# Performance work log

Hardware: AMD Instinct MI355X
Metric: run time of the kernel (lower is better)

Reference implementation:

```python
import jax, jax.numpy as jnp
import numpy as np

EPS = 1e-12  # F.normalize eps


def setup_inputs() -> dict:
    key = jax.random.key(0)
    ks = jax.random.split(key, 6)
    B, T, D = 8, 4096, 1024
    L, K, CD = 8, 1024, 16
    return {
        "z_e": jax.random.normal(ks[0], (B, T, D), jnp.float32),
        "Wd": jax.random.normal(ks[1], (L, CD, D), jnp.float32) * 0.02,
        "bd": jnp.zeros((L, CD), jnp.float32),
        "cb": jax.random.normal(ks[2], (L, K, CD), jnp.float32) * 0.02,
        "Wu": jax.random.normal(ks[3], (L, D, CD), jnp.float32) * 0.02,
        "bu": jnp.zeros((L, D), jnp.float32),
    }


def _l2norm(x):
    return x / jnp.maximum(jnp.linalg.norm(x, axis=-1, keepdims=True), EPS)


def reference(z_e, Wd, bd, cb, Wu, bu):
    """z_e: (B,T,D). Returns (z_q_concat, codes, commitment_loss, codebook_loss, entropy_loss)."""
    B, T, D = z_e.shape
    L, K, CD = cb.shape
    sg = jax.lax.stop_gradient
    residual = z_e
    zq_list, codes_list = [], []
    commit = jnp.asarray(0.0, z_e.dtype)
    cbl = jnp.asarray(0.0, z_e.dtype)
    for i in range(L):
        # proj_down: Linear(D -> CD), weight (CD, D)
        z_i = jnp.einsum('btd,cd->btc', residual, Wd[i]) + bd[i]  # (B,T,CD)
        flat = z_i.reshape(-1, CD)                                 # (N,CD)
        cb_i = cb[i]                                               # (K,CD)
        # L2-normalized lookup; argmin of euclidean cdist == argmin of squared dist
        zn, cbn = _l2norm(flat), _l2norm(cb_i)
        d2 = (jnp.sum(zn * zn, -1, keepdims=True)
              - 2.0 * (zn @ cbn.T)
              + jnp.sum(cbn * cbn, -1))                            # (N,K)
        codes = jnp.argmin(d2, axis=-1)                            # (N,)
        z_q = cb_i[codes].reshape(B, T, CD)                        # gather from RAW codebook
        commit = commit + jnp.mean((z_i - sg(z_q)) ** 2)
        cbl = cbl + jnp.mean((z_q - sg(z_i)) ** 2)
        zq_list.append(z_i + sg(z_q - z_i))                        # straight-through
        # residual update uses detached z_q; proj_up weight (D, CD)
        residual = residual - (jnp.einsum('btc,dc->btd', sg(z_q), Wu[i]) + bu[i])
        codes_list.append(codes.reshape(B, T))
    z_q_concat = jnp.concatenate(zq_list, axis=-1)                 # (B,T,L*CD)
    codes_all = jnp.stack(codes_list, axis=-1)                     # (B,T,L)
    entropy_loss = jnp.asarray(0.0, z_e.dtype)                     # entropy_loss_weight == 0
    return z_q_concat, codes_all, commit, cbl, entropy_loss
```

## Files before the change

### kernel.cpp

```cpp
#include <hip/hip_runtime.h>
#include <math.h>


#define TAU 3e-4f

#define WS_WACC   0
#define WS_HV64   64
#define WS_G64    2048
#define WS_CBN64  133120
#define WS_CBF    1247232
#define WS_G32    1902592
#define WS_HV32   1968128
#define WS_BMAT   1968640
#define WS_SBU    2492928

typedef __attribute__((ext_vector_type(8))) short short8v;
typedef __attribute__((ext_vector_type(4))) float f32x4;

__device__ __forceinline__ void gload_lds16(const void* g, void* l) {
    __builtin_amdgcn_global_load_lds(
        (const __attribute__((address_space(1))) void*)g,
        (__attribute__((address_space(3))) void*)l, 16, 0, 0);
}

__device__ __forceinline__ unsigned short bf16_rne(float x) {
    unsigned u = __float_as_uint(x);
    u += 0x7FFFu + ((u >> 16) & 1u);
    return (unsigned short)(u >> 16);
}
__device__ __forceinline__ float bf16_to_f32(unsigned short h) {
    return __uint_as_float(((unsigned)h) << 16);
}

__global__ void __launch_bounds__(256) rvq_prep1(
    const float* __restrict__ cb, const float* __restrict__ Wd,
    const float* __restrict__ bu,
    double* __restrict__ cbn64, unsigned short* __restrict__ cbf,
    float* __restrict__ Bmat, double* __restrict__ sbu,
    double* __restrict__ wacc)
{
    const int b = blockIdx.x, t = threadIdx.x;
    if (b < 32) {
        const int idx = b * 256 + t;
        const float* cp = cb + (size_t)idx * 16;
        double v[16]; double n = 0.0;
#pragma unroll
        for (int c = 0; c < 16; ++c) { v[c] = (double)cp[c]; n = fma(v[c], v[c], n); }
        const double iv = 1.0 / fmax(sqrt(n), 1e-12);
        double* r64 = cbn64 + (size_t)idx * 17;
        unsigned short* cf = cbf + (size_t)idx * 32;
        double c2 = 0.0;
#pragma unroll
        for (int c = 0; c < 16; ++c) {
            const double x = v[c] * iv;
            c2 = fma(x, x, c2);
            r64[c] = x;
            const float xf = (float)x;
            const unsigned short hh = bf16_rne(xf);
            cf[c] = hh;
            cf[16 + c] = bf16_rne(xf - bf16_to_f32(hh));
        }
        r64[16] = c2;
    } else if (b < 160) {
        const int ic = b - 32;
        const int d0 = t * 4;
        const float4 v = *(const float4*)(Wd + (size_t)ic * 1024 + d0);
        Bmat[(size_t)(d0 + 0) * 128 + ic] = v.x;
        Bmat[(size_t)(d0 + 1) * 128 + ic] = v.y;
        Bmat[(size_t)(d0 + 2) * 128 + ic] = v.z;
        Bmat[(size_t)(d0 + 3) * 128 + ic] = v.w;
    } else if (b < 192) {
        const int idx = b - 160;
        const int i = idx >> 2, d = (idx & 3) * 256 + t;
        double s = 0.0;
        for (int j = 0; j < i; ++j) s += (double)bu[j * 1024 + d];
        sbu[i * 1024 + d] = s;
    } else {
        if (t == 0) wacc[0] = 0.0;
    }
}

__global__ void __launch_bounds__(256) rvq_prep2(
    const float* __restrict__ Wu, const float* __restrict__ Wd,
    const float* __restrict__ bd, const double* __restrict__ sbu,
    double* __restrict__ G64, float* __restrict__ G32,
    double* __restrict__ hv64, float* __restrict__ hv32)
{
    __shared__ double sm2[1200];
    float* smf = (float*)sm2;
    const int b = blockIdx.x, t = threadIdx.x;
    if (b < 64) {
        const int j = b >> 3, i = b & 7;
        if (j >= i) return;
        float* Aus = smf;
        float* Bds = smf + 1280;
        const int a = t >> 4, bb = t & 15;
        double s = 0.0;
        for (int ch = 0; ch < 16; ++ch) {
            __syncthreads();
            {
                const int dd = t >> 2, a4 = (t & 3) * 4;
                const float4 v = *(const float4*)(Wu + (size_t)j * 16384
                                  + (size_t)(ch * 64 + dd) * 16 + a4);
                *(float4*)&Aus[dd * 20 + a4] = v;
                const int br = t >> 4, d4 = (t & 15) * 4;
                const float4 w = *(const float4*)(Wd + (size_t)i * 16384
                                  + (size_t)br * 1024 + ch * 64 + d4);
                *(float4*)&Bds[br * 68 + d4] = w;
            }
            __syncthreads();
#pragma unroll
            for (int dd = 0; dd < 64; ++dd)
                s = fma((double)Aus[dd * 20 + a], (double)Bds[bb * 68 + dd], s);
        }
        G64[(size_t)(j * 8 + i) * 256 + t] = s;
        G32[(size_t)(j * 8 + i) * 256 + t] = (float)s;
    } else {
        const int i = b - 64;
        const int dq = t >> 4, bb = t & 15;
        const double* sp = sbu + i * 1024 + dq * 64;
        const float*  wp = Wd + (size_t)i * 16384 + (size_t)bb * 1024 + dq * 64;
        double s = 0.0;
#pragma unroll
        for (int dd = 0; dd < 64; ++dd)
            s = fma(sp[dd], (double)wp[dd], s);
        sm2[dq * 20 + bb] = s;
        __syncthreads();
        if (t < 16) {
            double s2 = 0.0;
#pragma unroll
            for (int q = 0; q < 16; ++q) s2 += sm2[q * 20 + t];
            const double h = (double)bd[i * 16 + t] - s2;
            hv64[i * 16 + t] = h; hv32[i * 16 + t] = (float)h;
        }
    }
}

__global__ void __launch_bounds__(256, 4) rvq_main(
    const float* __restrict__ z_e, const float* __restrict__ Wd,
    const float* __restrict__ cb,
    const float* __restrict__ Bmat, const float* __restrict__ hv32,
    const double* __restrict__ hv64,
    const unsigned short* __restrict__ cbf, const double* __restrict__ cbn64,
    const float* __restrict__ G32, const double* __restrict__ G64,
    double* __restrict__ wacc,
    float* __restrict__ out0, float* __restrict__ out1)
{
    __shared__ __attribute__((aligned(16))) double stag_d[1312];
    __shared__ float ybuf[32 * 132];
    __shared__ float znbuf[32 * 20];
    __shared__ float candd[64], candd2[64];
    __shared__ int   candk[64];
    __shared__ float zqs[32 * 17];
    __shared__ int   bkhist[256];
    __shared__ int   bks[32], flist[32];
    __shared__ int   flagcnt;
    float* stag = reinterpret_cast<float*>(stag_d);

    const int t = threadIdx.x;
    const int tok0g = blockIdx.x * 32;

    {
        float* As = stag;
        float* Bs = stag + 576;
        const int tg2 = t >> 5, cg2 = t & 31;
        const int wid = t >> 6, lane = t & 63;
        float acc[4][4];
#pragma unroll
        for (int h = 0; h < 4; ++h)
#pragma unroll
            for (int x = 0; x < 4; ++x) acc[h][x] = 0.f;

#pragma unroll 1
        for (int ko = 0; ko < 64; ++ko) {
            const int k0 = ko * 16;
            __syncthreads();
            {
                const int m = t >> 3, kk2 = (t & 7) * 2;
                const float2 v = *(const float2*)(z_e +
                    (size_t)(tok0g + m) * 1024 + k0 + kk2);
                As[kk2 * 36 + m] = v.x;
                As[(kk2 + 1) * 36 + m] = v.y;
            }
            {
                const float* bsrc = Bmat + (size_t)k0 * 128 + wid * 512 + lane * 4;
                float* bdst = Bs + wid * 512;
                gload_lds16(bsrc, bdst);
                gload_lds16(bsrc + 256, bdst + 256);
            }
            __syncthreads();
#pragma unroll
            for (int kk = 0; kk < 16; ++kk) {
                const float4 a4 = *(const float4*)&As[kk * 36 + tg2 * 4];
                const float4 b4 = *(const float4*)&Bs[kk * 128 + cg2 * 4];
                acc[0][0] = fmaf(a4.x, b4.x, acc[0][0]);
                acc[0][1] = fmaf(a4.x, b4.y, acc[0][1]);
                acc[0][2] = fmaf(a4.x, b4.z, acc[0][2]);
                acc[0][3] = fmaf(a4.x, b4.w, acc[0][3]);
                acc[1][0] = fmaf(a4.y, b4.x, acc[1][0]);
                acc[1][1] = fmaf(a4.y, b4.y, acc[1][1]);
                acc[1][2] = fmaf(a4.y, b4.z, acc[1][2]);
                acc[1][3] = fmaf(a4.y, b4.w, acc[1][3]);
                acc[2][0] = fmaf(a4.z, b4.x, acc[2][0]);
                acc[2][1] = fmaf(a4.z, b4.y, acc[2][1]);
                acc[2][2] = fmaf(a4.z, b4.z, acc[2][2]);
                acc[2][3] = fmaf(a4.z, b4.w, acc[2][3]);
                acc[3][0] = fmaf(a4.w, b4.x, acc[3][0]);
                acc[3][1] = fmaf(a4.w, b4.y, acc[3][1]);
                acc[3][2] = fmaf(a4.w, b4.z, acc[3][2]);
                acc[3][3] = fmaf(a4.w, b4.w, acc[3][3]);
            }
        }
        const float4 hv = *(const float4*)(hv32 + cg2 * 4);
#pragma unroll
        for (int h = 0; h < 4; ++h) {
            float4 y4;
            y4.x = acc[h][0] + hv.x;
            y4.y = acc[h][1] + hv.y;
            y4.z = acc[h][2] + hv.z;
            y4.w = acc[h][3] + hv.w;
            *(float4*)&ybuf[(tg2 * 4 + h) * 132 + cg2 * 4] = y4;
        }
    }

    double lacc = 0.0;
    const int w = t >> 6, lane = t & 63;
    const int blk = lane >> 4, col = lane & 15;
    const int Tt = w & 1, Hh = w >> 1;
    const bool lolane = blk >= 2;
#pragma unroll 1
    for (int l = 0; l < 8; ++l) {
        __syncthreads();
        if (t < 32) {
            const float* yr = &ybuf[t * 132 + l * 16];
            float yv[16]; float n2 = 0.f;
#pragma unroll
            for (int c = 0; c < 16; ++c) { yv[c] = yr[c]; n2 = fmaf(yv[c], yv[c], n2); }
            const float iv = 1.0f / fmaxf(sqrtf(n2), 1e-12f);
            float* zp = &znbuf[t * 20];
#pragma unroll
            for (int c = 0; c < 16; ++c) zp[c] = yv[c] * iv;
        }
        __syncthreads();

        short8v afrag;
        {
            const float* zp = &znbuf[(Tt * 16 + col) * 20 + (blk & 1) * 8];
            const float4 z0 = *(const float4*)zp;
            const float4 z1 = *(const float4*)(zp + 4);
            const float zv[8] = {z0.x, z0.y, z0.z, z0.w, z1.x, z1.y, z1.z, z1.w};
#pragma unroll
            for (int i = 0; i < 8; ++i) {
                const float x = -2.f * zv[i];
                const unsigned short h = bf16_rne(x);
                const unsigned short v2 = lolane ? bf16_rne(x - bf16_to_f32(h)) : h;
                afrag[i] = (short)v2;
            }
        }

        float bs[4], bs2[4]; int bk[4];
#pragma unroll
        for (int r = 0; r < 4; ++r) { bs[r] = 1e30f; bs2[r] = 1e30f; bk[r] = -1; }
        const unsigned short* cbp = cbf + ((size_t)(l * 1024 + Hh * 512 + col)) * 32;
        const unsigned short* p1 = cbp + (blk & 1) * 8;
        const unsigned short* p2 = cbp + 16 + (blk & 1) * 8;
#pragma unroll 2
        for (int tile = 0; tile < 32; ++tile) {
            const short8v b1 = *(const short8v*)(p1 + tile * 512);
            short8v b2 = {};
            if (!lolane) b2 = *(const short8v*)(p2 + tile * 512);
            f32x4 acc = {0.f, 0.f, 0.f, 0.f};
            acc = __builtin_amdgcn_mfma_f32_16x16x32_bf16(afrag, b1, acc, 0, 0, 0);
            acc = __builtin_amdgcn_mfma_f32_16x16x32_bf16(afrag, b2, acc, 0, 0, 0);
            const int k = Hh * 512 + tile * 16 + col;
#pragma unroll
            for (int r = 0; r < 4; ++r) {
                const float s = acc[r];
                const bool wn = s < bs[r];
                bs2[r] = wn ? bs[r] : fminf(bs2[r], s);
                bk[r]  = wn ? k : bk[r];
                bs[r]  = wn ? s : bs[r];
            }
        }

#pragma unroll
        for (int m = 1; m <= 8; m <<= 1) {
#pragma unroll
            for (int r = 0; r < 4; ++r) {
                const float ob = __shfl_xor(bs[r], m);
                const float os = __shfl_xor(bs2[r], m);
                const int   ok = __shfl_xor(bk[r], m);
                const bool wn = (ob < bs[r]) || (ob == bs[r] && ok < bk[r]);
                const float loser = wn ? bs[r] : ob;
                bs2[r] = fminf(fminf(bs2[r], os), loser);
                bs[r]  = wn ? ob : bs[r];
                bk[r]  = wn ? ok : bk[r];
            }
        }
        if (t == 0) flagcnt = 0;
        if (col == 0) {
#pragma unroll
            for (int r = 0; r < 4; ++r) {
                const int tok = Tt * 16 + blk * 4 + r;
                candd [Hh * 32 + tok] = bs[r];
                candd2[Hh * 32 + tok] = bs2[r];
                candk [Hh * 32 + tok] = bk[r];
            }
        }
        __syncthreads();
        if (t < 32) {
            float best = 1e30f, sec = 1e30f; int bkk = -1;
#pragma unroll
            for (int c = 0; c < 2; ++c) {
                const float d  = candd [c * 32 + t];
                const float d2 = candd2[c * 32 + t];
                const int   k  = candk [c * 32 + t];
                const bool wn = (d < best) || (d == best && k < bkk);
                const float nw = fminf(sec, fminf(best, d2));
                const float nl = fminf(sec, d);
                sec  = wn ? nw : nl;
                bkk  = wn ? k : bkk;
                best = wn ? d : best;
            }
            bks[t] = bkk;
            const float* yr = &ybuf[t * 132 + l * 16];
            float n2 = 0.f;
#pragma unroll
            for (int c = 0; c < 16; ++c) n2 = fmaf(yr[c], yr[c], n2);
            if ((sec - best < TAU) || (n2 < 1e-3f)) {
                const int p = atomicAdd(&flagcnt, 1); flist[p] = t;
            }
        }
        __syncthreads();

        const int nf = flagcnt;
#pragma unroll 1
        for (int f = 0; f < nf; ++f) {
            const int tok = flist[f];
            double* rpd = stag_d;
            {
                const int c = t & 15, ch = t >> 4;
                const float* gz = z_e + (size_t)(tok0g + tok) * 1024 + ch * 64;
                const float* wp = Wd + ((size_t)l * 16 + c) * 1024 + ch * 64;
                double pd = 0.0;
                for (int dd = 0; dd < 64; ++dd)
                    pd = fma((double)gz[dd], (double)wp[dd], pd);
                rpd[c * 16 + ch] = pd;
            }
            __syncthreads();
            if (t < 16) {
                double y = hv64[l * 16 + t];
#pragma unroll
                for (int ch = 0; ch < 16; ++ch) y += rpd[t * 16 + ch];
                for (int j = 0; j < l; ++j) {
                    const int bkj = bkhist[tok * 8 + j];
                    const float* qv = cb + ((size_t)j * 1024 + bkj) * 16;
                    const double* gp = G64 + (size_t)(j * 8 + l) * 256 + t;
                    double s = 0.0;
#pragma unroll
                    for (int a = 0; a < 16; ++a)
                        s = fma((double)qv[a], gp[a * 16], s);
                    y -= s;
                }
                rpd[256 + t] = y;
            }
            __syncthreads();
            if (t == 0) {
                double n2 = 0.0;
#pragma unroll
                for (int c = 0; c < 16; ++c) n2 = fma(rpd[256 + c], rpd[256 + c], n2);
                const double iv = 1.0 / fmax(sqrt(n2), 1e-12);
#pragma unroll
                for (int c = 0; c < 16; ++c) rpd[272 + c] = rpd[256 + c] * iv;
            }
            __syncthreads();
            {
                double bd_ = 1e300; int bk_ = -1;
#pragma unroll
                for (int q = 0; q < 4; ++q) {
                    const int k = q * 256 + t;
                    const double* row = cbn64 + (size_t)(l * 1024 + k) * 17;
                    double dot = 0.0;
#pragma unroll
                    for (int c = 0; c < 16; ++c) dot = fma(row[c], rpd[272 + c], dot);
                    const double s = fma(-2.0, dot, row[16]);
                    if (s < bd_) { bd_ = s; bk_ = k; }
                }
                rpd[288 + t] = bd_;
                ((int*)&rpd[544])[t] = bk_;
            }
            __syncthreads();
            if (t == 0) {
                double bd_ = 1e300; int bk_ = -1;
                for (int i = 0; i < 256; ++i) {
                    const double d = rpd[288 + i];
                    const int k = ((int*)&rpd[544])[i];
                    if (d < bd_ || (d == bd_ && k < bk_)) { bd_ = d; bk_ = k; }
                }
                bks[tok] = bk_;
            }
            __syncthreads();
        }

        if (t < 32) {
            const int bk_ = bks[t];
            bkhist[t * 8 + l] = bk_;
            const float4* qp = (const float4*)(cb + ((size_t)l * 1024 + bk_) * 16);
            const float4 q0 = qp[0], q1 = qp[1], q2 = qp[2], q3 = qp[3];
            float* op = out0 + (size_t)(tok0g + t) * 128 + l * 16;
            ((float4*)op)[0] = q0; ((float4*)op)[1] = q1;
            ((float4*)op)[2] = q2; ((float4*)op)[3] = q3;
            out1[(size_t)(tok0g + t) * 8 + l] = (float)bk_;
            const float qf[16] = {q0.x,q0.y,q0.z,q0.w, q1.x,q1.y,q1.z,q1.w,
                                  q2.x,q2.y,q2.z,q2.w, q3.x,q3.y,q3.z,q3.w};
#pragma unroll
            for (int a = 0; a < 16; ++a) zqs[t * 17 + a] = qf[a];
            const float* yr = &ybuf[t * 132 + l * 16];
#pragma unroll
            for (int c = 0; c < 16; ++c) {
                const float d = yr[c] - qf[c];
                lacc += (double)d * (double)d;
            }
        }
        __syncthreads();

        if (l < 7) {
            {
                const int total = (7 - l) * 256;
                for (int idx = t; idx < total; idx += 256) {
                    const int ii = l + 1 + (idx >> 8);
                    stag[idx] = G32[(size_t)(l * 8 + ii) * 256 + (idx & 255)];
                }
            }
            __syncthreads();
            const int part = t >> 5, tok = t & 31;
            const int ii = l + 1 + part;
            if (ii < 8) {
                float zql[16];
#pragma unroll
                for (int a = 0; a < 16; ++a) zql[a] = zqs[tok * 17 + a];
                const float* gb = &stag[part * 256];
                float corr[16];
#pragma unroll
                for (int x = 0; x < 16; ++x) corr[x] = 0.f;
#pragma unroll
                for (int a = 0; a < 16; ++a) {
                    const float4 g0 = *(const float4*)&gb[a * 16];
                    const float4 g1 = *(const float4*)&gb[a * 16 + 4];
                    const float4 g2 = *(const float4*)&gb[a * 16 + 8];
                    const float4 g3 = *(const float4*)&gb[a * 16 + 12];
                    const float za = zql[a];
                    corr[0]  = fmaf(za, g0.x, corr[0]);  corr[1]  = fmaf(za, g0.y, corr[1]);
                    corr[2]  = fmaf(za, g0.z, corr[2]);  corr[3]  = fmaf(za, g0.w, corr[3]);
                    corr[4]  = fmaf(za, g1.x, corr[4]);  corr[5]  = fmaf(za, g1.y, corr[5]);
                    corr[6]  = fmaf(za, g1.z, corr[6]);  corr[7]  = fmaf(za, g1.w, corr[7]);
                    corr[8]  = fmaf(za, g2.x, corr[8]);  corr[9]  = fmaf(za, g2.y, corr[9]);
                    corr[10] = fmaf(za, g2.z, corr[10]); corr[11] = fmaf(za, g2.w, corr[11]);
                    corr[12] = fmaf(za, g3.x, corr[12]); corr[13] = fmaf(za, g3.y, corr[13]);
                    corr[14] = fmaf(za, g3.z, corr[14]); corr[15] = fmaf(za, g3.w, corr[15]);
                }
                float* yr = &ybuf[tok * 132 + ii * 16];
#pragma unroll
                for (int v = 0; v < 4; ++v) {
                    float4 y4 = *(float4*)&yr[v * 4];
                    y4.x -= corr[v * 4 + 0]; y4.y -= corr[v * 4 + 1];
                    y4.z -= corr[v * 4 + 2]; y4.w -= corr[v * 4 + 3];
                    *(float4*)&yr[v * 4] = y4;
                }
            }
        }
    }

    if (t < 64) {
#pragma unroll
        for (int off = 32; off > 0; off >>= 1) lacc += __shfl_down(lacc, off);
        if (t == 0) atomicAdd(wacc, lacc);
    }
}

__global__ void __launch_bounds__(64) rvq_fin(const double* __restrict__ wacc,
                                              float* __restrict__ lossp) {
    if (threadIdx.x == 0) {
        const float v = (float)(wacc[0] * (1.0 / 524288.0));
        lossp[0] = v; lossp[1] = v; lossp[2] = 0.0f;
    }
}

extern "C" void kernel_launch(void* const* d_in, const int* in_sizes, int n_in,
                              void* d_out, int out_size, void* d_ws, size_t ws_size,
                              hipStream_t stream) {
    (void)in_sizes; (void)n_in; (void)ws_size;
    const float* z_e = (const float*)d_in[0];
    const float* Wd  = (const float*)d_in[1];
    const float* bd  = (const float*)d_in[2];
    const float* cb  = (const float*)d_in[3];
    const float* Wu  = (const float*)d_in[4];
    const float* bu  = (const float*)d_in[5];

    float* out0  = (float*)d_out;
    float* out1  = out0 + (size_t)8 * 4096 * 128;
    float* lossp = out0 + (size_t)out_size - 3;

    char* ws = (char*)d_ws;
    double* wacc  = (double*)(ws + WS_WACC);
    double* hv64  = (double*)(ws + WS_HV64);
    double* G64   = (double*)(ws + WS_G64);
    double* cbn64 = (double*)(ws + WS_CBN64);
    unsigned short* cbf = (unsigned short*)(ws + WS_CBF);
    float*  G32   = (float*) (ws + WS_G32);
    float*  hv32  = (float*) (ws + WS_HV32);
    float*  Bmat  = (float*) (ws + WS_BMAT);
    double* sbu   = (double*)(ws + WS_SBU);

    rvq_prep1<<<193, 256, 0, stream>>>(cb, Wd, bu, cbn64, cbf, Bmat, sbu, wacc);
    rvq_prep2<<<72, 256, 0, stream>>>(Wu, Wd, bd, sbu, G64, G32, hv64, hv32);
    rvq_main<<<1024, 256, 0, stream>>>(z_e, Wd, cb, Bmat, hv32, hv64,
                                       cbf, cbn64, G32, G64, wacc, out0, out1);
    rvq_fin<<<1, 64, 0, stream>>>(wacc, lossp);
}
```

Before: 658.2 us.

## Use split-bf16 MFMA for projection GEMM, merge prep kernels, widen search tiling

Replaces the fp32 FMA LDS-tiled projection GEMM (z_e x Wd^T) with MFMA 16x16x32 bf16 using a three-product hi/lo split, which keeps near-fp32 accuracy. Wd is pre-packed into bf16 hi/lo fragments, and z_e is read directly from global memory with no LDS staging. The two prep kernels are merged into one launch, and the sbu prefix sum is computed inline. Each wave in the codebook search now handles both 16-token halves over 256 codes instead of one half over 512, which reuses B fragments and removes the znbuf normalization pass and one barrier. The split-bf16 GEMM may shift near-tie results slightly, and the direct global loads of z_e are uncoalesced per lane.

After: 622.5 us. 5.4% less time.

```diff
diff --git a/kernel.cpp b/kernel.cpp
--- a/kernel.cpp
+++ b/kernel.cpp
@@ -11,17 +11,11 @@
 #define WS_CBF    1247232
 #define WS_G32    1902592
 #define WS_HV32   1968128
-#define WS_BMAT   1968640
-#define WS_SBU    2492928
+#define WS_BF     1968640
+#define BF_LO_OFF 131072
 
 typedef __attribute__((ext_vector_type(8))) short short8v;
 typedef __attribute__((ext_vector_type(4))) float f32x4;
-
-__device__ __forceinline__ void gload_lds16(const void* g, void* l) {
-    __builtin_amdgcn_global_load_lds(
-        (const __attribute__((address_space(1))) void*)g,
-        (__attribute__((address_space(3))) void*)l, 16, 0, 0);
-}
 
 __device__ __forceinline__ unsigned short bf16_rne(float x) {
     unsigned u = __float_as_uint(x);
@@ -32,13 +26,18 @@
     return __uint_as_float(((unsigned)h) << 16);
 }
 
-__global__ void __launch_bounds__(256) rvq_prep1(
+__global__ void __launch_bounds__(256) rvq_prep(
     const float* __restrict__ cb, const float* __restrict__ Wd,
+    const float* __restrict__ Wu, const float* __restrict__ bd,
     const float* __restrict__ bu,
     double* __restrict__ cbn64, unsigned short* __restrict__ cbf,
-    float* __restrict__ Bmat, double* __restrict__ sbu,
+    unsigned short* __restrict__ Bf,
+    double* __restrict__ G64, float* __restrict__ G32,
+    double* __restrict__ hv64, float* __restrict__ hv32,
     double* __restrict__ wacc)
 {
+    __shared__ double sm2[1200];
+    float* smf = (float*)sm2;
     const int b = blockIdx.x, t = threadIdx.x;
     if (b < 32) {
         const int idx = b * 256 + t;
@@ -61,36 +60,25 @@
             cf[16 + c] = bf16_rne(xf - bf16_to_f32(hh));
         }
         r64[16] = c2;
+    } else if (b < 96) {
+        const int u = (b - 32) * 4 + (t >> 6);
+        const int lane = t & 63;
+        const int ks = u >> 3, ctg = u & 7;
+        const int ic = ctg * 16 + (lane & 15);
+        const int kb = ks * 32 + (lane >> 4) * 8;
+        const float* wp = Wd + (size_t)ic * 1024 + kb;
+        const float4 w0 = *(const float4*)wp;
+        const float4 w1 = *(const float4*)(wp + 4);
+        const float wv[8] = {w0.x, w0.y, w0.z, w0.w, w1.x, w1.y, w1.z, w1.w};
+        unsigned short* dst = Bf + ((size_t)(ks * 8 + ctg) * 64 + lane) * 8;
+#pragma unroll
+        for (int i = 0; i < 8; ++i) {
+            const unsigned short hh = bf16_rne(wv[i]);
+            dst[i] = hh;
+            dst[BF_LO_OFF + i] = bf16_rne(wv[i] - bf16_to_f32(hh));
+        }
     } else if (b < 160) {
-        const int ic = b - 32;
-        const int d0 = t * 4;
-        const float4 v = *(const float4*)(Wd + (size_t)ic * 1024 + d0);
-        Bmat[(size_t)(d0 + 0) * 128 + ic] = v.x;
-        Bmat[(size_t)(d0 + 1) * 128 + ic] = v.y;
-        Bmat[(size_t)(d0 + 2) * 128 + ic] = v.z;
-        Bmat[(size_t)(d0 + 3) * 128 + ic] = v.w;
-    } else if (b < 192) {
-        const int idx = b - 160;
-        const int i = idx >> 2, d = (idx & 3) * 256 + t;
-        double s = 0.0;
-        for (int j = 0; j < i; ++j) s += (double)bu[j * 1024 + d];
-        sbu[i * 1024 + d] = s;
-    } else {
-        if (t == 0) wacc[0] = 0.0;
-    }
-}
-
-__global__ void __launch_bounds__(256) rvq_prep2(
-    const float* __restrict__ Wu, const float* __restrict__ Wd,
-    const float* __restrict__ bd, const double* __restrict__ sbu,
-    double* __restrict__ G64, float* __restrict__ G32,
-    double* __restrict__ hv64, float* __restrict__ hv32)
-{
-    __shared__ double sm2[1200];
-    float* smf = (float*)sm2;
-    const int b = blockIdx.x, t = threadIdx.x;
-    if (b < 64) {
-        const int j = b >> 3, i = b & 7;
+        const int j = (b - 96) >> 3, i = (b - 96) & 7;
         if (j >= i) return;
         float* Aus = smf;
         float* Bds = smf + 1280;
@@ -115,15 +103,17 @@
         }
         G64[(size_t)(j * 8 + i) * 256 + t] = s;
         G32[(size_t)(j * 8 + i) * 256 + t] = (float)s;
-    } else {
-        const int i = b - 64;
+    } else if (b < 168) {
+        const int i = b - 160;
         const int dq = t >> 4, bb = t & 15;
-        const double* sp = sbu + i * 1024 + dq * 64;
-        const float*  wp = Wd + (size_t)i * 16384 + (size_t)bb * 1024 + dq * 64;
+        const float* wp = Wd + (size_t)i * 16384 + (size_t)bb * 1024 + dq * 64;
+        const float* bup = bu + dq * 64;
         double s = 0.0;
-#pragma unroll
-        for (int dd = 0; dd < 64; ++dd)
-            s = fma(sp[dd], (double)wp[dd], s);
+        for (int dd = 0; dd < 64; ++dd) {
+            double sb = 0.0;
+            for (int j = 0; j < i; ++j) sb += (double)bup[j * 1024 + dd];
+            s = fma(sb, (double)wp[dd], s);
+        }
         sm2[dq * 20 + bb] = s;
         __syncthreads();
         if (t < 16) {
@@ -133,24 +123,25 @@
             const double h = (double)bd[i * 16 + t] - s2;
             hv64[i * 16 + t] = h; hv32[i * 16 + t] = (float)h;
         }
+    } else {
+        if (t == 0) wacc[0] = 0.0;
     }
 }
 
 __global__ void __launch_bounds__(256, 4) rvq_main(
     const float* __restrict__ z_e, const float* __restrict__ Wd,
     const float* __restrict__ cb,
-    const float* __restrict__ Bmat, const float* __restrict__ hv32,
+    const unsigned short* __restrict__ Bf, const float* __restrict__ hv32,
     const double* __restrict__ hv64,
     const unsigned short* __restrict__ cbf, const double* __restrict__ cbn64,
     const float* __restrict__ G32, const double* __restrict__ G64,
     double* __restrict__ wacc,
     float* __restrict__ out0, float* __restrict__ out1)
 {
-    __shared__ __attribute__((aligned(16))) double stag_d[1312];
+    __shared__ __attribute__((aligned(16))) double stag_d[896];
     __shared__ float ybuf[32 * 132];
-    __shared__ float znbuf[32 * 20];
-    __shared__ float candd[64], candd2[64];
-    __shared__ int   candk[64];
+    __shared__ float candd[128], candd2[128];
+    __shared__ int   candk[128];
     __shared__ float zqs[32 * 17];
     __shared__ int   bkhist[256];
     __shared__ int   bks[32], flist[32];
@@ -159,159 +150,141 @@
 
     const int t = threadIdx.x;
     const int tok0g = blockIdx.x * 32;
+    const int wq = t >> 6, lane = t & 63;
+    const int blk = lane >> 4, col = lane & 15, kh = blk & 1;
+    const bool lolane = blk >= 2;
 
     {
-        float* As = stag;
-        float* Bs = stag + 576;
-        const int tg2 = t >> 5, cg2 = t & 31;
-        const int wid = t >> 6, lane = t & 63;
-        float acc[4][4];
-#pragma unroll
-        for (int h = 0; h < 4; ++h)
-#pragma unroll
-            for (int x = 0; x < 4; ++x) acc[h][x] = 0.f;
-
-#pragma unroll 1
-        for (int ko = 0; ko < 64; ++ko) {
-            const int k0 = ko * 16;
-            __syncthreads();
-            {
-                const int m = t >> 3, kk2 = (t & 7) * 2;
-                const float2 v = *(const float2*)(z_e +
-                    (size_t)(tok0g + m) * 1024 + k0 + kk2);
-                As[kk2 * 36 + m] = v.x;
-                As[(kk2 + 1) * 36 + m] = v.y;
-            }
-            {
-                const float* bsrc = Bmat + (size_t)k0 * 128 + wid * 512 + lane * 4;
-                float* bdst = Bs + wid * 512;
-                gload_lds16(bsrc, bdst);
-                gload_lds16(bsrc + 256, bdst + 256);
-            }
-            __syncthreads();
-#pragma unroll
-            for (int kk = 0; kk < 16; ++kk) {
-                const float4 a4 = *(const float4*)&As[kk * 36 + tg2 * 4];
-                const float4 b4 = *(const float4*)&Bs[kk * 128 + cg2 * 4];
-                acc[0][0] = fmaf(a4.x, b4.x, acc[0][0]);
-                acc[0][1] = fmaf(a4.x, b4.y, acc[0][1]);
-                acc[0][2] = fmaf(a4.x, b4.z, acc[0][2]);
-                acc[0][3] = fmaf(a4.x, b4.w, acc[0][3]);
-                acc[1][0] = fmaf(a4.y, b4.x, acc[1][0]);
-                acc[1][1] = fmaf(a4.y, b4.y, acc[1][1]);
-                acc[1][2] = fmaf(a4.y, b4.z, acc[1][2]);
-                acc[1][3] = fmaf(a4.y, b4.w, acc[1][3]);
-                acc[2][0] = fmaf(a4.z, b4.x, acc[2][0]);
-                acc[2][1] = fmaf(a4.z, b4.y, acc[2][1]);
-                acc[2][2] = fmaf(a4.z, b4.z, acc[2][2]);
-                acc[2][3] = fmaf(a4.z, b4.w, acc[2][3]);
-                acc[3][0] = fmaf(a4.w, b4.x, acc[3][0]);
-                acc[3][1] = fmaf(a4.w, b4.y, acc[3][1]);
-                acc[3][2] = fmaf(a4.w, b4.z, acc[3][2]);
-                acc[3][3] = fmaf(a4.w, b4.w, acc[3][3]);
-            }
-        }
-        const float4 hv = *(const float4*)(hv32 + cg2 * 4);
-#pragma unroll
-        for (int h = 0; h < 4; ++h) {
-            float4 y4;
-            y4.x = acc[h][0] + hv.x;
-            y4.y = acc[h][1] + hv.y;
-            y4.z = acc[h][2] + hv.z;
-            y4.w = acc[h][3] + hv.w;
-            *(float4*)&ybuf[(tg2 * 4 + h) * 132 + cg2 * 4] = y4;
+        const int Ch = wq >> 1, Tt = wq & 1;
+        const float* zrow = z_e + (size_t)(tok0g + Tt * 16 + col) * 1024 + blk * 8;
+        const unsigned short* bfh = Bf + ((size_t)(Ch * 4) * 64 + lane) * 8;
+        f32x4 acc[4];
+#pragma unroll
+        for (int ct = 0; ct < 4; ++ct) acc[ct] = (f32x4){0.f, 0.f, 0.f, 0.f};
+
+#pragma unroll 2
+        for (int ks = 0; ks < 32; ++ks) {
+            const float4 a0 = *(const float4*)(zrow + ks * 32);
+            const float4 a1 = *(const float4*)(zrow + ks * 32 + 4);
+            const float av[8] = {a0.x, a0.y, a0.z, a0.w, a1.x, a1.y, a1.z, a1.w};
+            short8v ah, al;
+#pragma unroll
+            for (int i = 0; i < 8; ++i) {
+                const unsigned short hh = bf16_rne(av[i]);
+                ah[i] = (short)hh;
+                al[i] = (short)bf16_rne(av[i] - bf16_to_f32(hh));
+            }
+            const unsigned short* bp = bfh + (size_t)ks * 4096;
+#pragma unroll
+            for (int ct = 0; ct < 4; ++ct) {
+                const short8v bh = *(const short8v*)(bp + ct * 512);
+                const short8v bl = *(const short8v*)(bp + BF_LO_OFF + ct * 512);
+                acc[ct] = __builtin_amdgcn_mfma_f32_16x16x32_bf16(ah, bh, acc[ct], 0, 0, 0);
+                acc[ct] = __builtin_amdgcn_mfma_f32_16x16x32_bf16(ah, bl, acc[ct], 0, 0, 0);
+                acc[ct] = __builtin_amdgcn_mfma_f32_16x16x32_bf16(al, bh, acc[ct], 0, 0, 0);
+            }
+        }
+#pragma unroll
+        for (int ct = 0; ct < 4; ++ct) {
+            const float hvv = hv32[Ch * 64 + ct * 16 + col];
+#pragma unroll
+            for (int r = 0; r < 4; ++r)
+                ybuf[(Tt * 16 + blk * 4 + r) * 132 + Ch * 64 + ct * 16 + col]
+                    = acc[ct][r] + hvv;
         }
     }
 
     double lacc = 0.0;
-    const int w = t >> 6, lane = t & 63;
-    const int blk = lane >> 4, col = lane & 15;
-    const int Tt = w & 1, Hh = w >> 1;
-    const bool lolane = blk >= 2;
+    const int q = wq;
 #pragma unroll 1
     for (int l = 0; l < 8; ++l) {
         __syncthreads();
-        if (t < 32) {
-            const float* yr = &ybuf[t * 132 + l * 16];
-            float yv[16]; float n2 = 0.f;
-#pragma unroll
-            for (int c = 0; c < 16; ++c) { yv[c] = yr[c]; n2 = fmaf(yv[c], yv[c], n2); }
+
+        short8v af[2];
+#pragma unroll
+        for (int h = 0; h < 2; ++h) {
+            const float* yp = &ybuf[(h * 16 + col) * 132 + l * 16 + kh * 8];
+            const float4 y0 = *(const float4*)yp;
+            const float4 y1 = *(const float4*)(yp + 4);
+            const float yv[8] = {y0.x, y0.y, y0.z, y0.w, y1.x, y1.y, y1.z, y1.w};
+            float p = 0.f;
+#pragma unroll
+            for (int i = 0; i < 8; ++i) p = fmaf(yv[i], yv[i], p);
+            const float n2 = p + __shfl_xor(p, 16);
             const float iv = 1.0f / fmaxf(sqrtf(n2), 1e-12f);
-            float* zp = &znbuf[t * 20];
-#pragma unroll
-            for (int c = 0; c < 16; ++c) zp[c] = yv[c] * iv;
-        }
-        __syncthreads();
-
-        short8v afrag;
-        {
-            const float* zp = &znbuf[(Tt * 16 + col) * 20 + (blk & 1) * 8];
-            const float4 z0 = *(const float4*)zp;
-            const float4 z1 = *(const float4*)(zp + 4);
-            const float zv[8] = {z0.x, z0.y, z0.z, z0.w, z1.x, z1.y, z1.z, z1.w};
 #pragma unroll
             for (int i = 0; i < 8; ++i) {
-                const float x = -2.f * zv[i];
-                const unsigned short h = bf16_rne(x);
-                const unsigned short v2 = lolane ? bf16_rne(x - bf16_to_f32(h)) : h;
-                afrag[i] = (short)v2;
-            }
-        }
-
-        float bs[4], bs2[4]; int bk[4];
-#pragma unroll
-        for (int r = 0; r < 4; ++r) { bs[r] = 1e30f; bs2[r] = 1e30f; bk[r] = -1; }
-        const unsigned short* cbp = cbf + ((size_t)(l * 1024 + Hh * 512 + col)) * 32;
-        const unsigned short* p1 = cbp + (blk & 1) * 8;
-        const unsigned short* p2 = cbp + 16 + (blk & 1) * 8;
+                const float x = -2.f * (yv[i] * iv);
+                const unsigned short hh = bf16_rne(x);
+                af[h][i] = (short)(lolane ? bf16_rne(x - bf16_to_f32(hh)) : hh);
+            }
+        }
+
+        float bs[2][4], bs2[2][4]; int bk[2][4];
+#pragma unroll
+        for (int h = 0; h < 2; ++h)
+#pragma unroll
+            for (int r = 0; r < 4; ++r) { bs[h][r] = 1e30f; bs2[h][r] = 1e30f; bk[h][r] = -1; }
+        const unsigned short* cbp = cbf + ((size_t)(l * 1024 + q * 256 + col)) * 32;
+        const unsigned short* p1 = cbp + kh * 8;
+        const unsigned short* p2 = cbp + 16 + kh * 8;
 #pragma unroll 2
-        for (int tile = 0; tile < 32; ++tile) {
+        for (int tile = 0; tile < 16; ++tile) {
             const short8v b1 = *(const short8v*)(p1 + tile * 512);
             short8v b2 = {};
             if (!lolane) b2 = *(const short8v*)(p2 + tile * 512);
-            f32x4 acc = {0.f, 0.f, 0.f, 0.f};
-            acc = __builtin_amdgcn_mfma_f32_16x16x32_bf16(afrag, b1, acc, 0, 0, 0);
-            acc = __builtin_amdgcn_mfma_f32_16x16x32_bf16(afrag, b2, acc, 0, 0, 0);
-            const int k = Hh * 512 + tile * 16 + col;
-#pragma unroll
-            for (int r = 0; r < 4; ++r) {
-                const float s = acc[r];
-                const bool wn = s < bs[r];
-                bs2[r] = wn ? bs[r] : fminf(bs2[r], s);
-                bk[r]  = wn ? k : bk[r];
-                bs[r]  = wn ? s : bs[r];
-            }
-        }
-
-#pragma unroll
-        for (int m = 1; m <= 8; m <<= 1) {
-#pragma unroll
-            for (int r = 0; r < 4; ++r) {
-                const float ob = __shfl_xor(bs[r], m);
-                const float os = __shfl_xor(bs2[r], m);
-                const int   ok = __shfl_xor(bk[r], m);
-                const bool wn = (ob < bs[r]) || (ob == bs[r] && ok < bk[r]);
-                const float loser = wn ? bs[r] : ob;
-                bs2[r] = fminf(fminf(bs2[r], os), loser);
-                bs[r]  = wn ? ob : bs[r];
-                bk[r]  = wn ? ok : bk[r];
-            }
-        }
+            f32x4 aa[2];
+            aa[0] = (f32x4){0.f, 0.f, 0.f, 0.f};
+            aa[0] = __builtin_amdgcn_mfma_f32_16x16x32_bf16(af[0], b1, aa[0], 0, 0, 0);
+            aa[0] = __builtin_amdgcn_mfma_f32_16x16x32_bf16(af[0], b2, aa[0], 0, 0, 0);
+            aa[1] = (f32x4){0.f, 0.f, 0.f, 0.f};
+            aa[1] = __builtin_amdgcn_mfma_f32_16x16x32_bf16(af[1], b1, aa[1], 0, 0, 0);
+            aa[1] = __builtin_amdgcn_mfma_f32_16x16x32_bf16(af[1], b2, aa[1], 0, 0, 0);
+            const int k = q * 256 + tile * 16 + col;
+#pragma unroll
+            for (int h = 0; h < 2; ++h)
+#pragma unroll
+                for (int r = 0; r < 4; ++r) {
+                    const float s = aa[h][r];
+                    const bool wn = s < bs[h][r];
+                    bs2[h][r] = wn ? bs[h][r] : fminf(bs2[h][r], s);
+                    bk[h][r]  = wn ? k : bk[h][r];
+                    bs[h][r]  = wn ? s : bs[h][r];
+                }
+        }
+
+#pragma unroll
+        for (int m = 1; m <= 8; m <<= 1)
+#pragma unroll
+            for (int h = 0; h < 2; ++h)
+#pragma unroll
+                for (int r = 0; r < 4; ++r) {
+                    const float ob = __shfl_xor(bs[h][r], m);
+                    const float os = __shfl_xor(bs2[h][r], m);
+                    const int   ok = __shfl_xor(bk[h][r], m);
+                    const bool wn = (ob < bs[h][r]) || (ob == bs[h][r] && ok < bk[h][r]);
+                    const float loser = wn ? bs[h][r] : ob;
+                    bs2[h][r] = fminf(fminf(bs2[h][r], os), loser);
+                    bs[h][r]  = wn ? ob : bs[h][r];
+                    bk[h][r]  = wn ? ok : bk[h][r];
+                }
         if (t == 0) flagcnt = 0;
         if (col == 0) {
 #pragma unroll
-            for (int r = 0; r < 4; ++r) {
-                const int tok = Tt * 16 + blk * 4 + r;
-                candd [Hh * 32 + tok] = bs[r];
-                candd2[Hh * 32 + tok] = bs2[r];
-                candk [Hh * 32 + tok] = bk[r];
-            }
+            for (int h = 0; h < 2; ++h)
+#pragma unroll
+                for (int r = 0; r < 4; ++r) {
+                    const int tok = h * 16 + blk * 4 + r;
+                    candd [q * 32 + tok] = bs[h][r];
+                    candd2[q * 32 + tok] = bs2[h][r];
+                    candk [q * 32 + tok] = bk[h][r];
+                }
         }
         __syncthreads();
         if (t < 32) {
             float best = 1e30f, sec = 1e30f; int bkk = -1;
 #pragma unroll
-            for (int c = 0; c < 2; ++c) {
+            for (int c = 0; c < 4; ++c) {
                 const float d  = candd [c * 32 + t];
                 const float d2 = candd2[c * 32 + t];
                 const int   k  = candk [c * 32 + t];
@@ -377,8 +350,8 @@
             {
                 double bd_ = 1e300; int bk_ = -1;
 #pragma unroll
-                for (int q = 0; q < 4; ++q) {
-                    const int k = q * 256 + t;
+                for (int qq = 0; qq < 4; ++qq) {
+                    const int k = qq * 256 + t;
                     const double* row = cbn64 + (size_t)(l * 1024 + k) * 17;
                     double dot = 0.0;
 #pragma unroll
@@ -509,12 +482,11 @@
     unsigned short* cbf = (unsigned short*)(ws + WS_CBF);
     float*  G32   = (float*) (ws + WS_G32);
     float*  hv32  = (float*) (ws + WS_HV32);
-    float*  Bmat  = (float*) (ws + WS_BMAT);
-    double* sbu   = (double*)(ws + WS_SBU);
-
-    rvq_prep1<<<193, 256, 0, stream>>>(cb, Wd, bu, cbn64, cbf, Bmat, sbu, wacc);
-    rvq_prep2<<<72, 256, 0, stream>>>(Wu, Wd, bd, sbu, G64, G32, hv64, hv32);
-    rvq_main<<<1024, 256, 0, stream>>>(z_e, Wd, cb, Bmat, hv32, hv64,
+    unsigned short* Bf = (unsigned short*)(ws + WS_BF);
+
+    rvq_prep<<<169, 256, 0, stream>>>(cb, Wd, Wu, bd, bu, cbn64, cbf, Bf,
+                                      G64, G32, hv64, hv32, wacc);
+    rvq_main<<<1024, 256, 0, stream>>>(z_e, Wd, cb, Bf, hv32, hv64,
                                        cbf, cbn64, G32, G64, wacc, out0, out1);
     rvq_fin<<<1, 64, 0, stream>>>(wacc, lossp);
 }
```
